# Kernel optimization log

Measured on AMD Instinct MI355X. Metric: run time of the kernel, lower is better.

Reference implementation:

```python
import jax, jax.numpy as jnp
import numpy as np

N_NODES = 50000
N_EDGES = 800000
F_IN = 128
HEADS = 2
C_HID = 64
N_GRAPHS = 32
NEG_SLOPE = 0.2
LP_LAYERS = 2
LP_ALPHA = 0.5


def gatv2_conv(x, src, dst, W_l, W_r, att, bias):
    """GATv2Conv (concat=True), edge_attr=None, self-loops already in src/dst."""
    H, C = att.shape
    N = x.shape[0]
    xl = (x @ W_l).reshape(N, H, C)  # source-side transform (x_j)
    xr = (x @ W_r).reshape(N, H, C)  # target-side transform (x_i)
    xj = xl[src]                      # [E,H,C]
    e = jax.nn.leaky_relu(xr[dst] + xj, NEG_SLOPE)
    logits = jnp.einsum('ehc,hc->eh', e, att)  # [E,H]
    # segment softmax over incoming edges of each target node
    m = jax.ops.segment_max(logits, dst, num_segments=N)
    m = jnp.where(jnp.isfinite(m), m, 0.0)
    p = jnp.exp(logits - m[dst])
    s = jax.ops.segment_sum(p, dst, num_segments=N)
    alpha = p / (s[dst] + 1e-16)
    out = jax.ops.segment_sum(xj * alpha[:, :, None], dst, num_segments=N)
    return out.reshape(N, H * C) + bias


def label_prop(y, src, dst):
    """PyG LabelPropagation: sym gcn_norm (no self-loops), clamp(0,1) post-step."""
    N = y.shape[0]
    ones = jnp.ones(src.shape[0], dtype=y.dtype)
    deg = jax.ops.segment_sum(ones, dst, num_segments=N)
    dinv = jnp.where(deg > 0, jax.lax.rsqrt(jnp.maximum(deg, 1.0)), 0.0)
    w = (dinv[src] * dinv[dst])[:, None]
    res = (1.0 - LP_ALPHA) * y
    out = y
    for _ in range(LP_LAYERS):
        out = LP_ALPHA * jax.ops.segment_sum(out[src] * w, dst, num_segments=N) + res
        out = jnp.clip(out, 0.0, 1.0)
    return out


def setup_inputs() -> dict:
    key = jax.random.key(0)
    ks = jax.random.split(key, 16)
    HC = HEADS * C_HID

    def glorot(k, shape):
        lim = np.sqrt(6.0 / (shape[0] + shape[-1]))
        return jax.random.uniform(k, shape, jnp.float32, -lim, lim)

    x = jax.random.normal(ks[0], (N_NODES, F_IN), jnp.float32)
    edge_index = jax.random.randint(ks[1], (2, N_EDGES), 0, N_NODES, jnp.int32)
    batch = jnp.sort(jax.random.randint(ks[2], (N_NODES,), 0, N_GRAPHS, jnp.int32))
    return {
        'x': x, 'edge_index': edge_index, 'batch': batch,
        'W_l1': glorot(ks[3], (F_IN, HC)), 'W_r1': glorot(ks[4], (F_IN, HC)),
        'att1': glorot(ks[5], (HEADS, C_HID)), 'b1': jnp.zeros((HC,), jnp.float32),
        'W_l2': glorot(ks[6], (HC, HC)), 'W_r2': glorot(ks[7], (HC, HC)),
        'att2': glorot(ks[8], (HEADS, C_HID)), 'b2': jnp.zeros((HC,), jnp.float32),
        'mlp_W1': glorot(ks[9], (F_IN + 2 * HC, 256)), 'mlp_b1': jnp.zeros((256,), jnp.float32),
        'mlp_W2': glorot(ks[10], (256, 128)), 'mlp_b2': jnp.zeros((128,), jnp.float32),
    }


def reference(x, edge_index, batch, W_l1, W_r1, att1, b1, W_l2, W_r2, att2, b2,
              mlp_W1, mlp_b1, mlp_W2, mlp_b2):
    N = x.shape[0]
    src, dst = edge_index[0], edge_index[1]
    # GATv2Conv adds self-loops by default
    loop = jnp.arange(N, dtype=src.dtype)
    src_sl = jnp.concatenate([src, loop])
    dst_sl = jnp.concatenate([dst, loop])

    h0 = x
    h1 = jax.nn.elu(gatv2_conv(h0, src_sl, dst_sl, W_l1, W_r1, att1, b1))
    h1 = label_prop(h1, src, dst)
    h2 = jax.nn.elu(gatv2_conv(h1, src_sl, dst_sl, W_l2, W_r2, att2, b2))
    h2 = label_prop(h2, src, dst)

    combined = jnp.concatenate([h0, h1, h2], axis=-1)  # [N, 384]
    # global mean pool over graphs
    sums = jax.ops.segment_sum(combined, batch, num_segments=N_GRAPHS)
    cnts = jax.ops.segment_sum(jnp.ones((N,), combined.dtype), batch, num_segments=N_GRAPHS)
    g = sums / jnp.maximum(cnts, 1.0)[:, None]  # [G, 384]

    h = jax.nn.relu(g @ mlp_W1 + mlp_b1)  # dropout is identity in eval
    return h @ mlp_W2 + mlp_b2
```

## Files before the change

### kernel.cpp

```cpp
#include <hip/hip_runtime.h>
#include <math.h>

#define FDIM 128
#define NEG_SLOPE 0.2f
#define LP_ALPHA 0.5f
#define NGRAPHS 32
#define POOLF 384
#define MLP_H 256
#define OUT_F 128
#define POOL_CH 8

#define LRELU(z) ((z) > 0.0f ? (z) : NEG_SLOPE * (z))
#define RFL(v) __builtin_amdgcn_readfirstlane(v)

__global__ void count_deg_k(const int* __restrict__ dst, int* __restrict__ deg, int E) {
    int e = blockIdx.x * blockDim.x + threadIdx.x;
    if (e < E) atomicAdd(&deg[dst[e]], 1);
}

__global__ __launch_bounds__(256) void scan_part_k(const int* __restrict__ deg,
                                                   int* __restrict__ tileSum, int N) {
    int b = blockIdx.x, t = threadIdx.x;
    int base = b * 1024 + t * 4;
    int v = 0;
    if (base + 3 < N) { int4 d = *(const int4*)(deg + base); v = d.x + d.y + d.z + d.w; }
    else if (base < N) {
        v = deg[base];
        if (base + 1 < N) v += deg[base + 1];
        if (base + 2 < N) v += deg[base + 2];
    }
#pragma unroll
    for (int off = 32; off > 0; off >>= 1) v += __shfl_xor(v, off, 64);
    __shared__ int ws[4];
    if ((t & 63) == 0) ws[t >> 6] = v;
    __syncthreads();
    if (t == 0) tileSum[b] = ws[0] + ws[1] + ws[2] + ws[3];
}

__global__ void scan_tiles_k(const int* __restrict__ tileSum, int* __restrict__ tileOff, int nt) {
    int t = threadIdx.x;
    int v = (t < nt) ? tileSum[t] : 0;
    int incl = v;
#pragma unroll
    for (int off = 1; off < 64; off <<= 1) {
        int u = __shfl_up(incl, off, 64);
        if (t >= off) incl += u;
    }
    if (t < nt) tileOff[t] = incl - v;
}

__global__ __launch_bounds__(256) void scan_write_k(const int* __restrict__ deg,
                                                    const int* __restrict__ tileOff,
                                                    int* __restrict__ row_ptr,
                                                    float* __restrict__ dinv, int N, int E) {
    int b = blockIdx.x, t = threadIdx.x;
    int base = b * 1024 + t * 4;
    int d0 = 0, d1 = 0, d2 = 0, d3 = 0;
    if (base + 3 < N) { int4 d = *(const int4*)(deg + base); d0 = d.x; d1 = d.y; d2 = d.z; d3 = d.w; }
    else if (base < N) {
        d0 = deg[base];
        if (base + 1 < N) d1 = deg[base + 1];
        if (base + 2 < N) d2 = deg[base + 2];
    }
    int lsum = d0 + d1 + d2 + d3;
    int lane = t & 63, wv = t >> 6;
    int incl = lsum;
#pragma unroll
    for (int off = 1; off < 64; off <<= 1) {
        int u = __shfl_up(incl, off, 64);
        if (lane >= off) incl += u;
    }
    __shared__ int wsum[4];
    if (lane == 63) wsum[wv] = incl;
    __syncthreads();
    int woff = 0;
#pragma unroll
    for (int k = 0; k < 4; ++k) if (k < wv) woff += wsum[k];
    int off0 = tileOff[b] + woff + (incl - lsum);
    if (base < N)     { row_ptr[base]     = off0;                dinv[base]     = d0 > 0 ? 1.0f / sqrtf((float)d0) : 0.0f; }
    if (base + 1 < N) { row_ptr[base + 1] = off0 + d0;           dinv[base + 1] = d1 > 0 ? 1.0f / sqrtf((float)d1) : 0.0f; }
    if (base + 2 < N) { row_ptr[base + 2] = off0 + d0 + d1;      dinv[base + 2] = d2 > 0 ? 1.0f / sqrtf((float)d2) : 0.0f; }
    if (base + 3 < N) { row_ptr[base + 3] = off0 + d0 + d1 + d2; dinv[base + 3] = d3 > 0 ? 1.0f / sqrtf((float)d3) : 0.0f; }
    if (b == 0 && t == 0) row_ptr[N] = E;
}

__global__ void scatter_k(const int* __restrict__ src, const int* __restrict__ dst,
                          const int* __restrict__ row_ptr, int* __restrict__ fill,
                          const float* __restrict__ dinv, int2* __restrict__ elist, int E) {
    int e = blockIdx.x * blockDim.x + threadIdx.x;
    if (e >= E) return;
    int d = dst[e], s = src[e];
    int pos = atomicAdd(&fill[d], 1);
    unsigned long long v = (unsigned int)s |
                           ((unsigned long long)(unsigned int)__float_as_int(dinv[s]) << 32);
    __builtin_nontemporal_store(v, (unsigned long long*)&elist[row_ptr[d] + pos]);
}

__global__ void gbound_k(const int* __restrict__ batch, int* __restrict__ gb, int N) {
    int g = threadIdx.x;
    if (g > NGRAPHS) return;
    int lo = 0, hi = N;
    while (lo < hi) {
        int mid = (lo + hi) >> 1;
        if (batch[mid] < g) lo = mid + 1; else hi = mid;
    }
    gb[g] = lo;
}

__global__ __launch_bounds__(256) void gemm128x2_k(const float* __restrict__ X,
                                                   const float* __restrict__ Wl,
                                                   const float* __restrict__ Wr,
                                                   float* __restrict__ Yl,
                                                   float* __restrict__ Yr, int N) {
    __shared__ float Xs[FDIM][68];
    int t = threadIdx.x;
    int r0 = blockIdx.x * 64;
    for (int idx = t; idx < 64 * FDIM; idx += 256) {
        int k = idx & 127, r = idx >> 7;
        int row = r0 + r;
        Xs[k][r] = (row < N) ? X[(size_t)row * FDIM + k] : 0.0f;
    }
    __syncthreads();
    int tr = t >> 5;
    int tc = t & 31;
    float accl[8][4] = {{0.f}}, accr[8][4] = {{0.f}};
#pragma unroll 2
    for (int k = 0; k < FDIM; ++k) {
        float4 bl = *(const float4*)(Wl + k * FDIM + tc * 4);
        float4 br = *(const float4*)(Wr + k * FDIM + tc * 4);
        float4 a0 = *(const float4*)(&Xs[k][tr * 8]);
        float4 a1 = *(const float4*)(&Xs[k][tr * 8 + 4]);
        float av[8] = {a0.x, a0.y, a0.z, a0.w, a1.x, a1.y, a1.z, a1.w};
#pragma unroll
        for (int r = 0; r < 8; ++r) {
            accl[r][0] = fmaf(av[r], bl.x, accl[r][0]);
            accl[r][1] = fmaf(av[r], bl.y, accl[r][1]);
            accl[r][2] = fmaf(av[r], bl.z, accl[r][2]);
            accl[r][3] = fmaf(av[r], bl.w, accl[r][3]);
            accr[r][0] = fmaf(av[r], br.x, accr[r][0]);
            accr[r][1] = fmaf(av[r], br.y, accr[r][1]);
            accr[r][2] = fmaf(av[r], br.z, accr[r][2]);
            accr[r][3] = fmaf(av[r], br.w, accr[r][3]);
        }
    }
#pragma unroll
    for (int r = 0; r < 8; ++r) {
        int row = r0 + tr * 8 + r;
        if (row < N) {
            *(float4*)(Yl + (size_t)row * FDIM + tc * 4) =
                make_float4(accl[r][0], accl[r][1], accl[r][2], accl[r][3]);
            *(float4*)(Yr + (size_t)row * FDIM + tc * 4) =
                make_float4(accr[r][0], accr[r][1], accr[r][2], accr[r][3]);
        }
    }
}

__global__ __launch_bounds__(256) void gat_pull_k(const float* __restrict__ xl,
                                                  const float* __restrict__ xr,
                                                  const int* __restrict__ row_ptr,
                                                  const int2* __restrict__ elist,
                                                  const float* __restrict__ att,
                                                  const float* __restrict__ bias,
                                                  float* __restrict__ out, int N) {
    int wid = threadIdx.x >> 6;
    int lane = threadIdx.x & 63;
    int i = blockIdx.x * 4 + wid;
    if (i >= N) return;
    float2 at  = *(const float2*)(att + 2 * lane);
    size_t ibase = (size_t)i * FDIM + 2 * lane;
    float2 xrv   = *(const float2*)(xr + ibase);
    float2 xself = *(const float2*)(xl + ibase);

    auto hred = [](float v) {
        v += __shfl_xor(v, 16, 64);
        v += __shfl_xor(v, 8, 64);
        v += __shfl_xor(v, 4, 64);
        v += __shfl_xor(v, 2, 64);
        v += __shfl_xor(v, 1, 64);
        return v;
    };

    float lself = hred(LRELU(xrv.x + xself.x) * at.x + LRELU(xrv.y + xself.y) * at.y);
    float m0 = lself, s0 = 1.0f, a0x = xself.x, a0y = xself.y;
    float m1 = -INFINITY, s1 = 0.0f, a1x = 0.0f, a1y = 0.0f;

    int beg = row_ptr[i], end = row_ptr[i + 1];
    int p = beg;
    for (; p + 3 < end; p += 4) {
        int j0 = RFL(elist[p].x);
        int j1 = RFL(elist[p + 1].x);
        int j2 = RFL(elist[p + 2].x);
        int j3 = RFL(elist[p + 3].x);
        float2 x0 = *(const float2*)(xl + (size_t)j0 * FDIM + 2 * lane);
        float2 x1 = *(const float2*)(xl + (size_t)j1 * FDIM + 2 * lane);
        float2 x2 = *(const float2*)(xl + (size_t)j2 * FDIM + 2 * lane);
        float2 x3 = *(const float2*)(xl + (size_t)j3 * FDIM + 2 * lane);
        float l0 = hred(LRELU(xrv.x + x0.x) * at.x + LRELU(xrv.y + x0.y) * at.y);
        float l1 = hred(LRELU(xrv.x + x1.x) * at.x + LRELU(xrv.y + x1.y) * at.y);
        float l2 = hred(LRELU(xrv.x + x2.x) * at.x + LRELU(xrv.y + x2.y) * at.y);
        float l3 = hred(LRELU(xrv.x + x3.x) * at.x + LRELU(xrv.y + x3.y) * at.y);
        { float mn = fmaxf(m0, l0); float sc = __expf(m0 - mn), pe = __expf(l0 - mn);
          s0 = fmaf(s0, sc, pe); a0x = fmaf(a0x, sc, pe * x0.x); a0y = fmaf(a0y, sc, pe * x0.y); m0 = mn; }
        { float mn = fmaxf(m1, l1); float sc = __expf(m1 - mn), pe = __expf(l1 - mn);
          s1 = fmaf(s1, sc, pe); a1x = fmaf(a1x, sc, pe * x1.x); a1y = fmaf(a1y, sc, pe * x1.y); m1 = mn; }
        { float mn = fmaxf(m0, l2); float sc = __expf(m0 - mn), pe = __expf(l2 - mn);
          s0 = fmaf(s0, sc, pe); a0x = fmaf(a0x, sc, pe * x2.x); a0y = fmaf(a0y, sc, pe * x2.y); m0 = mn; }
        { float mn = fmaxf(m1, l3); float sc = __expf(m1 - mn), pe = __expf(l3 - mn);
          s1 = fmaf(s1, sc, pe); a1x = fmaf(a1x, sc, pe * x3.x); a1y = fmaf(a1y, sc, pe * x3.y); m1 = mn; }
    }
    for (; p < end; ++p) {
        int j0 = RFL(elist[p].x);
        float2 x0 = *(const float2*)(xl + (size_t)j0 * FDIM + 2 * lane);
        float l0 = hred(LRELU(xrv.x + x0.x) * at.x + LRELU(xrv.y + x0.y) * at.y);
        float mn = fmaxf(m0, l0); float sc = __expf(m0 - mn), pe = __expf(l0 - mn);
        s0 = fmaf(s0, sc, pe); a0x = fmaf(a0x, sc, pe * x0.x); a0y = fmaf(a0y, sc, pe * x0.y); m0 = mn;
    }
    float mn = fmaxf(m0, m1);
    float c0 = __expf(m0 - mn);
    float c1 = (m1 == -INFINITY) ? 0.0f : __expf(m1 - mn);
    float s = fmaf(s0, c0, s1 * c1) + 1e-16f;
    float rx = (a0x * c0 + a1x * c1) / s;
    float ry = (a0y * c0 + a1y * c1) / s;
    float2 bv = *(const float2*)(bias + 2 * lane);
    float zx = rx + bv.x, zy = ry + bv.y;
    float2 o;
    o.x = (zx > 0.0f) ? zx : (__expf(zx) - 1.0f);
    o.y = (zy > 0.0f) ? zy : (__expf(zy) - 1.0f);
    *(float2*)(out + ibase) = o;
}

__global__ __launch_bounds__(256) void lp_pull_k(const float* __restrict__ y,
                                                 const float* __restrict__ cur,
                                                 float* __restrict__ nxt,
                                                 const int* __restrict__ row_ptr,
                                                 const int2* __restrict__ elist,
                                                 const float* __restrict__ dinv, int N) {
    int wid = threadIdx.x >> 6, lane = threadIdx.x & 63;
    int i = blockIdx.x * 4 + wid;
    if (i >= N) return;
    int beg = row_ptr[i], end = row_ptr[i + 1];
    float ax0 = 0.f, ay0 = 0.f, ax1 = 0.f, ay1 = 0.f;
    float ax2 = 0.f, ay2 = 0.f, ax3 = 0.f, ay3 = 0.f;
    float ax4 = 0.f, ay4 = 0.f, ax5 = 0.f, ay5 = 0.f;
    float ax6 = 0.f, ay6 = 0.f, ax7 = 0.f, ay7 = 0.f;
    int p = beg;
    for (; p + 7 < end; p += 8) {
        int2 e0 = elist[p + 0], e1 = elist[p + 1], e2 = elist[p + 2], e3 = elist[p + 3];
        int2 e4 = elist[p + 4], e5 = elist[p + 5], e6 = elist[p + 6], e7 = elist[p + 7];
        int j0 = RFL(e0.x); float w0 = __int_as_float(RFL(e0.y));
        int j1 = RFL(e1.x); float w1 = __int_as_float(RFL(e1.y));
        int j2 = RFL(e2.x); float w2 = __int_as_float(RFL(e2.y));
        int j3 = RFL(e3.x); float w3 = __int_as_float(RFL(e3.y));
        int j4 = RFL(e4.x); float w4 = __int_as_float(RFL(e4.y));
        int j5 = RFL(e5.x); float w5 = __int_as_float(RFL(e5.y));
        int j6 = RFL(e6.x); float w6 = __int_as_float(RFL(e6.y));
        int j7 = RFL(e7.x); float w7 = __int_as_float(RFL(e7.y));
        float2 v0 = *(const float2*)(cur + (size_t)j0 * FDIM + 2 * lane);
        float2 v1 = *(const float2*)(cur + (size_t)j1 * FDIM + 2 * lane);
        float2 v2 = *(const float2*)(cur + (size_t)j2 * FDIM + 2 * lane);
        float2 v3 = *(const float2*)(cur + (size_t)j3 * FDIM + 2 * lane);
        float2 v4 = *(const float2*)(cur + (size_t)j4 * FDIM + 2 * lane);
        float2 v5 = *(const float2*)(cur + (size_t)j5 * FDIM + 2 * lane);
        float2 v6 = *(const float2*)(cur + (size_t)j6 * FDIM + 2 * lane);
        float2 v7 = *(const float2*)(cur + (size_t)j7 * FDIM + 2 * lane);
        ax0 = fmaf(w0, v0.x, ax0); ay0 = fmaf(w0, v0.y, ay0);
        ax1 = fmaf(w1, v1.x, ax1); ay1 = fmaf(w1, v1.y, ay1);
        ax2 = fmaf(w2, v2.x, ax2); ay2 = fmaf(w2, v2.y, ay2);
        ax3 = fmaf(w3, v3.x, ax3); ay3 = fmaf(w3, v3.y, ay3);
        ax4 = fmaf(w4, v4.x, ax4); ay4 = fmaf(w4, v4.y, ay4);
        ax5 = fmaf(w5, v5.x, ax5); ay5 = fmaf(w5, v5.y, ay5);
        ax6 = fmaf(w6, v6.x, ax6); ay6 = fmaf(w6, v6.y, ay6);
        ax7 = fmaf(w7, v7.x, ax7); ay7 = fmaf(w7, v7.y, ay7);
    }
    for (; p < end; ++p) {
        int2 e0 = elist[p];
        int j0 = RFL(e0.x); float w0 = __int_as_float(RFL(e0.y));
        float2 v0 = *(const float2*)(cur + (size_t)j0 * FDIM + 2 * lane);
        ax0 = fmaf(w0, v0.x, ax0); ay0 = fmaf(w0, v0.y, ay0);
    }
    float sx = ((ax0 + ax1) + (ax2 + ax3)) + ((ax4 + ax5) + (ax6 + ax7));
    float sy = ((ay0 + ay1) + (ay2 + ay3)) + ((ay4 + ay5) + (ay6 + ay7));
    float di = dinv[i];
    float2 yv = *(const float2*)(y + (size_t)i * FDIM + 2 * lane);
    float vx = LP_ALPHA * (di * sx) + (1.0f - LP_ALPHA) * yv.x;
    float vy = LP_ALPHA * (di * sy) + (1.0f - LP_ALPHA) * yv.y;
    float2 o;
    o.x = fminf(fmaxf(vx, 0.f), 1.f);
    o.y = fminf(fmaxf(vy, 0.f), 1.f);
    *(float2*)(nxt + (size_t)i * FDIM + 2 * lane) = o;
}

__global__ void pool_part_k(const float* __restrict__ x, const float* __restrict__ h1,
                            const float* __restrict__ h2, const int* __restrict__ gb,
                            float* __restrict__ part) {
    int g = blockIdx.x, si = blockIdx.y, ch = blockIdx.z;
    int t = threadIdx.x;
    const float* s = (si == 0) ? x : ((si == 1) ? h1 : h2);
    int n0g = gb[g], n1g = gb[g + 1];
    int len = n1g - n0g;
    int per = (len + POOL_CH - 1) / POOL_CH;
    int n0 = n0g + ch * per;
    int n1 = min(n0 + per, n1g);
    float acc = 0.0f;
    for (int n = n0; n < n1; ++n) acc += s[(size_t)n * FDIM + t];
    part[(((g * 3 + si) << 3) + ch) * FDIM + t] = acc;
}

__global__ void mlp1_k(const float* __restrict__ part, const int* __restrict__ gb,
                       const float* __restrict__ W1, const float* __restrict__ b1,
                       float* __restrict__ h) {
    int g = blockIdx.x;
    int t = threadIdx.x;
    __shared__ float gm[POOLF];
    int cnt = gb[g + 1] - gb[g];
    float inv = 1.0f / fmaxf((float)cnt, 1.0f);
    for (int f = t; f < POOLF; f += 256) {
        int si = f >> 7, fl = f & 127;
        float s = 0.0f;
#pragma unroll
        for (int c = 0; c < POOL_CH; ++c)
            s += part[(((g * 3 + si) << 3) + c) * FDIM + fl];
        gm[f] = s * inv;
    }
    __syncthreads();
    float acc = b1[t];
    for (int k = 0; k < POOLF; ++k) acc = fmaf(gm[k], W1[k * MLP_H + t], acc);
    h[g * MLP_H + t] = fmaxf(acc, 0.0f);
}

__global__ void mlp2_k(const float* __restrict__ h, const float* __restrict__ W2,
                       const float* __restrict__ b2, float* __restrict__ out) {
    int g = blockIdx.x;
    int t = threadIdx.x;
    __shared__ float hs[MLP_H];
    for (int k = t; k < MLP_H; k += 128) hs[k] = h[g * MLP_H + k];
    __syncthreads();
    float acc = b2[t];
    for (int k = 0; k < MLP_H; ++k) acc = fmaf(hs[k], W2[k * OUT_F + t], acc);
    out[g * OUT_F + t] = acc;
}

extern "C" void kernel_launch(void* const* d_in, const int* in_sizes, int n_in,
                              void* d_out, int out_size, void* d_ws, size_t ws_size,
                              hipStream_t stream) {
    const float* x    = (const float*)d_in[0];
    const int*   ei   = (const int*)d_in[1];
    const int*   batch= (const int*)d_in[2];
    const float* W_l1 = (const float*)d_in[3];
    const float* W_r1 = (const float*)d_in[4];
    const float* att1 = (const float*)d_in[5];
    const float* b1   = (const float*)d_in[6];
    const float* W_l2 = (const float*)d_in[7];
    const float* W_r2 = (const float*)d_in[8];
    const float* att2 = (const float*)d_in[9];
    const float* b2   = (const float*)d_in[10];
    const float* mW1  = (const float*)d_in[11];
    const float* mb1  = (const float*)d_in[12];
    const float* mW2  = (const float*)d_in[13];
    const float* mb2  = (const float*)d_in[14];
    float* out = (float*)d_out;

    const int N = in_sizes[2];
    const int E = in_sizes[1] / 2;
    const int* src = ei;
    const int* dst = ei + E;

    char* w = (char*)d_ws;
    auto alloc = [&](size_t bytes) -> char* {
        char* p = w;
        w += (bytes + 255) & ~(size_t)255;
        return p;
    };
    float* bufA = (float*)alloc((size_t)N * FDIM * 4);
    float* bufB = (float*)alloc((size_t)N * FDIM * 4);
    float* bufC = (float*)alloc((size_t)N * FDIM * 4);
    float* bufD = (float*)alloc((size_t)N * FDIM * 4);
    int* deg     = (int*)alloc((size_t)N * 4);
    int* fill    = (int*)alloc((size_t)N * 4);
    int* row_lp  = (int*)alloc((size_t)(N + 1) * 4);
    int2* elist  = (int2*)alloc((size_t)E * 8);
    float* dinv  = (float*)alloc((size_t)N * 4);
    int* gb      = (int*)alloc((size_t)(NGRAPHS + 1) * 4);
    int* tileSum = (int*)alloc((size_t)64 * 4);
    int* tileOff = (int*)alloc((size_t)64 * 4);
    float* part  = (float*)alloc((size_t)NGRAPHS * 3 * POOL_CH * FDIM * 4);
    float* mlp_h = (float*)alloc((size_t)NGRAPHS * MLP_H * 4);

    const int TB = 256;
    int gE = (E + TB - 1) / TB;
    int nTiles = (N + 1023) / 1024;

    hipMemsetAsync(deg, 0, (size_t)N * 4, stream);
    hipMemsetAsync(fill, 0, (size_t)N * 4, stream);
    count_deg_k<<<gE, TB, 0, stream>>>(dst, deg, E);
    gbound_k<<<1, 64, 0, stream>>>(batch, gb, N);
    scan_part_k<<<nTiles, 256, 0, stream>>>(deg, tileSum, N);
    scan_tiles_k<<<1, 64, 0, stream>>>(tileSum, tileOff, nTiles);
    scan_write_k<<<nTiles, 256, 0, stream>>>(deg, tileOff, row_lp, dinv, N, E);
    scatter_k<<<gE, TB, 0, stream>>>(src, dst, row_lp, fill, dinv, elist, E);

    int gGemm = (N + 63) / 64;
    int gWave = (N + 3) / 4;

    gemm128x2_k<<<gGemm, 256, 0, stream>>>(x, W_l1, W_r1, bufA, bufB, N);
    gat_pull_k<<<gWave, 256, 0, stream>>>(bufA, bufB, row_lp, elist, att1, b1, bufC, N);
    lp_pull_k<<<gWave, 256, 0, stream>>>(bufC, bufC, bufA, row_lp, elist, dinv, N);
    lp_pull_k<<<gWave, 256, 0, stream>>>(bufC, bufA, bufC, row_lp, elist, dinv, N);

    gemm128x2_k<<<gGemm, 256, 0, stream>>>(bufC, W_l2, W_r2, bufA, bufB, N);
    gat_pull_k<<<gWave, 256, 0, stream>>>(bufA, bufB, row_lp, elist, att2, b2, bufD, N);
    lp_pull_k<<<gWave, 256, 0, stream>>>(bufD, bufD, bufA, row_lp, elist, dinv, N);
    lp_pull_k<<<gWave, 256, 0, stream>>>(bufD, bufA, bufD, row_lp, elist, dinv, N);

    pool_part_k<<<dim3(NGRAPHS, 3, POOL_CH), 128, 0, stream>>>(x, bufC, bufD, gb, part);

    mlp1_k<<<NGRAPHS, 256, 0, stream>>>(part, gb, mW1, mb1, mlp_h);
    mlp2_k<<<NGRAPHS, 128, 0, stream>>>(mlp_h, mW2, mb2, out);
}
```

Before: 773.5 us.

## Split each wave into two half-waves processing separate edges with float4 gathers

The GAT and label-propagation pull kernels now give each 32-lane half of a wave its own set of edges, with each lane loading float4 feature slices. The halves' online-softmax or sum partials are merged with a cross-half shuffle at the end. This doubles the number of independent row gathers in flight per wave and widens each load, at the cost of extra shuffles, predicated tail handling and one idle half during the store. Separately, the scatter step now uses a cursor array initialised with the row offsets, which removes one memset and the row_ptr lookup.

```diff
diff --git a/kernel.cpp b/kernel.cpp
--- a/kernel.cpp
+++ b/kernel.cpp
@@ -11,7 +11,6 @@
 #define POOL_CH 8
 
 #define LRELU(z) ((z) > 0.0f ? (z) : NEG_SLOPE * (z))
-#define RFL(v) __builtin_amdgcn_readfirstlane(v)
 
 __global__ void count_deg_k(const int* __restrict__ dst, int* __restrict__ deg, int E) {
     int e = blockIdx.x * blockDim.x + threadIdx.x;
@@ -52,6 +51,7 @@
 __global__ __launch_bounds__(256) void scan_write_k(const int* __restrict__ deg,
                                                     const int* __restrict__ tileOff,
                                                     int* __restrict__ row_ptr,
+                                                    int* __restrict__ cursor,
                                                     float* __restrict__ dinv, int N, int E) {
     int b = blockIdx.x, t = threadIdx.x;
     int base = b * 1024 + t * 4;
@@ -77,23 +77,27 @@
 #pragma unroll
     for (int k = 0; k < 4; ++k) if (k < wv) woff += wsum[k];
     int off0 = tileOff[b] + woff + (incl - lsum);
-    if (base < N)     { row_ptr[base]     = off0;                dinv[base]     = d0 > 0 ? 1.0f / sqrtf((float)d0) : 0.0f; }
-    if (base + 1 < N) { row_ptr[base + 1] = off0 + d0;           dinv[base + 1] = d1 > 0 ? 1.0f / sqrtf((float)d1) : 0.0f; }
-    if (base + 2 < N) { row_ptr[base + 2] = off0 + d0 + d1;      dinv[base + 2] = d2 > 0 ? 1.0f / sqrtf((float)d2) : 0.0f; }
-    if (base + 3 < N) { row_ptr[base + 3] = off0 + d0 + d1 + d2; dinv[base + 3] = d3 > 0 ? 1.0f / sqrtf((float)d3) : 0.0f; }
+    if (base < N)     { row_ptr[base]     = off0;                cursor[base]     = off0;
+                        dinv[base]     = d0 > 0 ? 1.0f / sqrtf((float)d0) : 0.0f; }
+    if (base + 1 < N) { row_ptr[base + 1] = off0 + d0;           cursor[base + 1] = off0 + d0;
+                        dinv[base + 1] = d1 > 0 ? 1.0f / sqrtf((float)d1) : 0.0f; }
+    if (base + 2 < N) { row_ptr[base + 2] = off0 + d0 + d1;      cursor[base + 2] = off0 + d0 + d1;
+                        dinv[base + 2] = d2 > 0 ? 1.0f / sqrtf((float)d2) : 0.0f; }
+    if (base + 3 < N) { row_ptr[base + 3] = off0 + d0 + d1 + d2; cursor[base + 3] = off0 + d0 + d1 + d2;
+                        dinv[base + 3] = d3 > 0 ? 1.0f / sqrtf((float)d3) : 0.0f; }
     if (b == 0 && t == 0) row_ptr[N] = E;
 }
 
 __global__ void scatter_k(const int* __restrict__ src, const int* __restrict__ dst,
-                          const int* __restrict__ row_ptr, int* __restrict__ fill,
-                          const float* __restrict__ dinv, int2* __restrict__ elist, int E) {
+                          int* __restrict__ cursor, const float* __restrict__ dinv,
+                          int2* __restrict__ elist, int E) {
     int e = blockIdx.x * blockDim.x + threadIdx.x;
     if (e >= E) return;
     int d = dst[e], s = src[e];
-    int pos = atomicAdd(&fill[d], 1);
+    int pos = atomicAdd(&cursor[d], 1);
     unsigned long long v = (unsigned int)s |
                            ((unsigned long long)(unsigned int)__float_as_int(dinv[s]) << 32);
-    __builtin_nontemporal_store(v, (unsigned long long*)&elist[row_ptr[d] + pos]);
+    __builtin_nontemporal_store(v, (unsigned long long*)&elist[pos]);
 }
 
 __global__ void gbound_k(const int* __restrict__ batch, int* __restrict__ gb, int N) {
@@ -164,15 +168,18 @@
                                                   float* __restrict__ out, int N) {
     int wid = threadIdx.x >> 6;
     int lane = threadIdx.x & 63;
+    int half = lane >> 5;
+    int lh = lane & 31;
     int i = blockIdx.x * 4 + wid;
     if (i >= N) return;
-    float2 at  = *(const float2*)(att + 2 * lane);
-    size_t ibase = (size_t)i * FDIM + 2 * lane;
-    float2 xrv   = *(const float2*)(xr + ibase);
-    float2 xself = *(const float2*)(xl + ibase);
-
-    auto hred = [](float v) {
-        v += __shfl_xor(v, 16, 64);
+    float4 at = *(const float4*)(att + 4 * lh);
+    size_t ibase = (size_t)i * FDIM + 4 * lh;
+    float4 xrv = *(const float4*)(xr + ibase);
+    float4 xs  = *(const float4*)(xl + ibase);
+
+    auto qdot = [&](float4 xv) {
+        float v = LRELU(xrv.x + xv.x) * at.x + LRELU(xrv.y + xv.y) * at.y
+                + LRELU(xrv.z + xv.z) * at.z + LRELU(xrv.w + xv.w) * at.w;
         v += __shfl_xor(v, 8, 64);
         v += __shfl_xor(v, 4, 64);
         v += __shfl_xor(v, 2, 64);
@@ -180,53 +187,73 @@
         return v;
     };
 
-    float lself = hred(LRELU(xrv.x + xself.x) * at.x + LRELU(xrv.y + xself.y) * at.y);
-    float m0 = lself, s0 = 1.0f, a0x = xself.x, a0y = xself.y;
-    float m1 = -INFINITY, s1 = 0.0f, a1x = 0.0f, a1y = 0.0f;
+    float lself = qdot(xs);
+    float m0 = half ? -INFINITY : lself;
+    float s0 = half ? 0.0f : 1.0f;
+    float4 a0 = half ? make_float4(0.f, 0.f, 0.f, 0.f) : xs;
+    float m1 = -INFINITY, s1 = 0.0f;
+    float4 a1 = make_float4(0.f, 0.f, 0.f, 0.f);
 
     int beg = row_ptr[i], end = row_ptr[i + 1];
-    int p = beg;
-    for (; p + 3 < end; p += 4) {
-        int j0 = RFL(elist[p].x);
-        int j1 = RFL(elist[p + 1].x);
-        int j2 = RFL(elist[p + 2].x);
-        int j3 = RFL(elist[p + 3].x);
-        float2 x0 = *(const float2*)(xl + (size_t)j0 * FDIM + 2 * lane);
-        float2 x1 = *(const float2*)(xl + (size_t)j1 * FDIM + 2 * lane);
-        float2 x2 = *(const float2*)(xl + (size_t)j2 * FDIM + 2 * lane);
-        float2 x3 = *(const float2*)(xl + (size_t)j3 * FDIM + 2 * lane);
-        float l0 = hred(LRELU(xrv.x + x0.x) * at.x + LRELU(xrv.y + x0.y) * at.y);
-        float l1 = hred(LRELU(xrv.x + x1.x) * at.x + LRELU(xrv.y + x1.y) * at.y);
-        float l2 = hred(LRELU(xrv.x + x2.x) * at.x + LRELU(xrv.y + x2.y) * at.y);
-        float l3 = hred(LRELU(xrv.x + x3.x) * at.x + LRELU(xrv.y + x3.y) * at.y);
-        { float mn = fmaxf(m0, l0); float sc = __expf(m0 - mn), pe = __expf(l0 - mn);
-          s0 = fmaf(s0, sc, pe); a0x = fmaf(a0x, sc, pe * x0.x); a0y = fmaf(a0y, sc, pe * x0.y); m0 = mn; }
-        { float mn = fmaxf(m1, l1); float sc = __expf(m1 - mn), pe = __expf(l1 - mn);
-          s1 = fmaf(s1, sc, pe); a1x = fmaf(a1x, sc, pe * x1.x); a1y = fmaf(a1y, sc, pe * x1.y); m1 = mn; }
-        { float mn = fmaxf(m0, l2); float sc = __expf(m0 - mn), pe = __expf(l2 - mn);
-          s0 = fmaf(s0, sc, pe); a0x = fmaf(a0x, sc, pe * x2.x); a0y = fmaf(a0y, sc, pe * x2.y); m0 = mn; }
-        { float mn = fmaxf(m1, l3); float sc = __expf(m1 - mn), pe = __expf(l3 - mn);
-          s1 = fmaf(s1, sc, pe); a1x = fmaf(a1x, sc, pe * x3.x); a1y = fmaf(a1y, sc, pe * x3.y); m1 = mn; }
-    }
-    for (; p < end; ++p) {
-        int j0 = RFL(elist[p].x);
-        float2 x0 = *(const float2*)(xl + (size_t)j0 * FDIM + 2 * lane);
-        float l0 = hred(LRELU(xrv.x + x0.x) * at.x + LRELU(xrv.y + x0.y) * at.y);
-        float mn = fmaxf(m0, l0); float sc = __expf(m0 - mn), pe = __expf(l0 - mn);
-        s0 = fmaf(s0, sc, pe); a0x = fmaf(a0x, sc, pe * x0.x); a0y = fmaf(a0y, sc, pe * x0.y); m0 = mn;
-    }
-    float mn = fmaxf(m0, m1);
-    float c0 = __expf(m0 - mn);
-    float c1 = (m1 == -INFINITY) ? 0.0f : __expf(m1 - mn);
-    float s = fmaf(s0, c0, s1 * c1) + 1e-16f;
-    float rx = (a0x * c0 + a1x * c1) / s;
-    float ry = (a0y * c0 + a1y * c1) / s;
-    float2 bv = *(const float2*)(bias + 2 * lane);
-    float zx = rx + bv.x, zy = ry + bv.y;
-    float2 o;
-    o.x = (zx > 0.0f) ? zx : (__expf(zx) - 1.0f);
-    o.y = (zy > 0.0f) ? zy : (__expf(zy) - 1.0f);
-    *(float2*)(out + ibase) = o;
+    for (int p = beg; p < end; p += 4) {
+        int i0 = p + half, i1 = p + 2 + half;
+        bool v0 = i0 < end, v1 = i1 < end;
+        int j0 = elist[min(i0, end - 1)].x;
+        int j1 = elist[min(i1, end - 1)].x;
+        float4 x0 = *(const float4*)(xl + (size_t)j0 * FDIM + 4 * lh);
+        float4 x1 = *(const float4*)(xl + (size_t)j1 * FDIM + 4 * lh);
+        float l0 = qdot(x0);
+        float l1 = qdot(x1);
+        if (v0) {
+            float mn = fmaxf(m0, l0);
+            float sc = __expf(m0 - mn), pe = __expf(l0 - mn);
+            s0 = fmaf(s0, sc, pe);
+            a0.x = fmaf(a0.x, sc, pe * x0.x); a0.y = fmaf(a0.y, sc, pe * x0.y);
+            a0.z = fmaf(a0.z, sc, pe * x0.z); a0.w = fmaf(a0.w, sc, pe * x0.w);
+            m0 = mn;
+        }
+        if (v1) {
+            float mn = fmaxf(m1, l1);
+            float sc = __expf(m1 - mn), pe = __expf(l1 - mn);
+            s1 = fmaf(s1, sc, pe);
+            a1.x = fmaf(a1.x, sc, pe * x1.x); a1.y = fmaf(a1.y, sc, pe * x1.y);
+            a1.z = fmaf(a1.z, sc, pe * x1.z); a1.w = fmaf(a1.w, sc, pe * x1.w);
+            m1 = mn;
+        }
+    }
+    {
+        float mn = fmaxf(m0, m1);
+        float c0 = (m0 == -INFINITY) ? 0.0f : __expf(m0 - mn);
+        float c1 = (m1 == -INFINITY) ? 0.0f : __expf(m1 - mn);
+        s0 = s0 * c0 + s1 * c1;
+        a0.x = a0.x * c0 + a1.x * c1; a0.y = a0.y * c0 + a1.y * c1;
+        a0.z = a0.z * c0 + a1.z * c1; a0.w = a0.w * c0 + a1.w * c1;
+        m0 = mn;
+    }
+    {
+        float pm = __shfl_xor(m0, 32, 64);
+        float ps = __shfl_xor(s0, 32, 64);
+        float px = __shfl_xor(a0.x, 32, 64), py = __shfl_xor(a0.y, 32, 64);
+        float pz = __shfl_xor(a0.z, 32, 64), pw = __shfl_xor(a0.w, 32, 64);
+        float mn = fmaxf(m0, pm);
+        float c0 = (m0 == -INFINITY) ? 0.0f : __expf(m0 - mn);
+        float c1 = (pm == -INFINITY) ? 0.0f : __expf(pm - mn);
+        s0 = s0 * c0 + ps * c1;
+        a0.x = a0.x * c0 + px * c1; a0.y = a0.y * c0 + py * c1;
+        a0.z = a0.z * c0 + pz * c1; a0.w = a0.w * c0 + pw * c1;
+    }
+    if (half == 0) {
+        float inv = 1.0f / (s0 + 1e-16f);
+        float4 bv = *(const float4*)(bias + 4 * lh);
+        float zx = a0.x * inv + bv.x, zy = a0.y * inv + bv.y;
+        float zz = a0.z * inv + bv.z, zw = a0.w * inv + bv.w;
+        float4 o;
+        o.x = (zx > 0.0f) ? zx : (__expf(zx) - 1.0f);
+        o.y = (zy > 0.0f) ? zy : (__expf(zy) - 1.0f);
+        o.z = (zz > 0.0f) ? zz : (__expf(zz) - 1.0f);
+        o.w = (zw > 0.0f) ? zw : (__expf(zw) - 1.0f);
+        *(float4*)(out + ibase) = o;
+    }
 }
 
 __global__ __launch_bounds__(256) void lp_pull_k(const float* __restrict__ y,
@@ -236,58 +263,54 @@
                                                  const int2* __restrict__ elist,
                                                  const float* __restrict__ dinv, int N) {
     int wid = threadIdx.x >> 6, lane = threadIdx.x & 63;
+    int half = lane >> 5, lh = lane & 31;
     int i = blockIdx.x * 4 + wid;
     if (i >= N) return;
     int beg = row_ptr[i], end = row_ptr[i + 1];
-    float ax0 = 0.f, ay0 = 0.f, ax1 = 0.f, ay1 = 0.f;
-    float ax2 = 0.f, ay2 = 0.f, ax3 = 0.f, ay3 = 0.f;
-    float ax4 = 0.f, ay4 = 0.f, ax5 = 0.f, ay5 = 0.f;
-    float ax6 = 0.f, ay6 = 0.f, ax7 = 0.f, ay7 = 0.f;
-    int p = beg;
-    for (; p + 7 < end; p += 8) {
-        int2 e0 = elist[p + 0], e1 = elist[p + 1], e2 = elist[p + 2], e3 = elist[p + 3];
-        int2 e4 = elist[p + 4], e5 = elist[p + 5], e6 = elist[p + 6], e7 = elist[p + 7];
-        int j0 = RFL(e0.x); float w0 = __int_as_float(RFL(e0.y));
-        int j1 = RFL(e1.x); float w1 = __int_as_float(RFL(e1.y));
-        int j2 = RFL(e2.x); float w2 = __int_as_float(RFL(e2.y));
-        int j3 = RFL(e3.x); float w3 = __int_as_float(RFL(e3.y));
-        int j4 = RFL(e4.x); float w4 = __int_as_float(RFL(e4.y));
-        int j5 = RFL(e5.x); float w5 = __int_as_float(RFL(e5.y));
-        int j6 = RFL(e6.x); float w6 = __int_as_float(RFL(e6.y));
-        int j7 = RFL(e7.x); float w7 = __int_as_float(RFL(e7.y));
-        float2 v0 = *(const float2*)(cur + (size_t)j0 * FDIM + 2 * lane);
-        float2 v1 = *(const float2*)(cur + (size_t)j1 * FDIM + 2 * lane);
-        float2 v2 = *(const float2*)(cur + (size_t)j2 * FDIM + 2 * lane);
-        float2 v3 = *(const float2*)(cur + (size_t)j3 * FDIM + 2 * lane);
-        float2 v4 = *(const float2*)(cur + (size_t)j4 * FDIM + 2 * lane);
-        float2 v5 = *(const float2*)(cur + (size_t)j5 * FDIM + 2 * lane);
-        float2 v6 = *(const float2*)(cur + (size_t)j6 * FDIM + 2 * lane);
-        float2 v7 = *(const float2*)(cur + (size_t)j7 * FDIM + 2 * lane);
-        ax0 = fmaf(w0, v0.x, ax0); ay0 = fmaf(w0, v0.y, ay0);
-        ax1 = fmaf(w1, v1.x, ax1); ay1 = fmaf(w1, v1.y, ay1);
-        ax2 = fmaf(w2, v2.x, ax2); ay2 = fmaf(w2, v2.y, ay2);
-        ax3 = fmaf(w3, v3.x, ax3); ay3 = fmaf(w3, v3.y, ay3);
-        ax4 = fmaf(w4, v4.x, ax4); ay4 = fmaf(w4, v4.y, ay4);
-        ax5 = fmaf(w5, v5.x, ax5); ay5 = fmaf(w5, v5.y, ay5);
-        ax6 = fmaf(w6, v6.x, ax6); ay6 = fmaf(w6, v6.y, ay6);
-        ax7 = fmaf(w7, v7.x, ax7); ay7 = fmaf(w7, v7.y, ay7);
-    }
-    for (; p < end; ++p) {
-        int2 e0 = elist[p];
-        int j0 = RFL(e0.x); float w0 = __int_as_float(RFL(e0.y));
-        float2 v0 = *(const float2*)(cur + (size_t)j0 * FDIM + 2 * lane);
-        ax0 = fmaf(w0, v0.x, ax0); ay0 = fmaf(w0, v0.y, ay0);
-    }
-    float sx = ((ax0 + ax1) + (ax2 + ax3)) + ((ax4 + ax5) + (ax6 + ax7));
-    float sy = ((ay0 + ay1) + (ay2 + ay3)) + ((ay4 + ay5) + (ay6 + ay7));
-    float di = dinv[i];
-    float2 yv = *(const float2*)(y + (size_t)i * FDIM + 2 * lane);
-    float vx = LP_ALPHA * (di * sx) + (1.0f - LP_ALPHA) * yv.x;
-    float vy = LP_ALPHA * (di * sy) + (1.0f - LP_ALPHA) * yv.y;
-    float2 o;
-    o.x = fminf(fmaxf(vx, 0.f), 1.f);
-    o.y = fminf(fmaxf(vy, 0.f), 1.f);
-    *(float2*)(nxt + (size_t)i * FDIM + 2 * lane) = o;
+    float4 a0 = make_float4(0.f, 0.f, 0.f, 0.f), a1 = a0, a2 = a0, a3 = a0;
+    for (int p = beg; p < end; p += 8) {
+        int i0 = p + half, i1 = p + 2 + half, i2 = p + 4 + half, i3 = p + 6 + half;
+        int2 e0 = elist[min(i0, end - 1)];
+        int2 e1 = elist[min(i1, end - 1)];
+        int2 e2 = elist[min(i2, end - 1)];
+        int2 e3 = elist[min(i3, end - 1)];
+        float w0 = (i0 < end) ? __int_as_float(e0.y) : 0.0f;
+        float w1 = (i1 < end) ? __int_as_float(e1.y) : 0.0f;
+        float w2 = (i2 < end) ? __int_as_float(e2.y) : 0.0f;
+        float w3 = (i3 < end) ? __int_as_float(e3.y) : 0.0f;
+        float4 x0 = *(const float4*)(cur + (size_t)e0.x * FDIM + 4 * lh);
+        float4 x1 = *(const float4*)(cur + (size_t)e1.x * FDIM + 4 * lh);
+        float4 x2 = *(const float4*)(cur + (size_t)e2.x * FDIM + 4 * lh);
+        float4 x3 = *(const float4*)(cur + (size_t)e3.x * FDIM + 4 * lh);
+        a0.x = fmaf(w0, x0.x, a0.x); a0.y = fmaf(w0, x0.y, a0.y);
+        a0.z = fmaf(w0, x0.z, a0.z); a0.w = fmaf(w0, x0.w, a0.w);
+        a1.x = fmaf(w1, x1.x, a1.x); a1.y = fmaf(w1, x1.y, a1.y);
+        a1.z = fmaf(w1, x1.z, a1.z); a1.w = fmaf(w1, x1.w, a1.w);
+        a2.x = fmaf(w2, x2.x, a2.x); a2.y = fmaf(w2, x2.y, a2.y);
+        a2.z = fmaf(w2, x2.z, a2.z); a2.w = fmaf(w2, x2.w, a2.w);
+        a3.x = fmaf(w3, x3.x, a3.x); a3.y = fmaf(w3, x3.y, a3.y);
+        a3.z = fmaf(w3, x3.z, a3.z); a3.w = fmaf(w3, x3.w, a3.w);
+    }
+    float4 a;
+    a.x = (a0.x + a1.x) + (a2.x + a3.x);
+    a.y = (a0.y + a1.y) + (a2.y + a3.y);
+    a.z = (a0.z + a1.z) + (a2.z + a3.z);
+    a.w = (a0.w + a1.w) + (a2.w + a3.w);
+    a.x += __shfl_xor(a.x, 32, 64);
+    a.y += __shfl_xor(a.y, 32, 64);
+    a.z += __shfl_xor(a.z, 32, 64);
+    a.w += __shfl_xor(a.w, 32, 64);
+    if (half == 0) {
+        float di = dinv[i];
+        size_t ibase = (size_t)i * FDIM + 4 * lh;
+        float4 yv = *(const float4*)(y + ibase);
+        float4 o;
+        o.x = fminf(fmaxf(fmaf(LP_ALPHA * di, a.x, (1.0f - LP_ALPHA) * yv.x), 0.f), 1.f);
+        o.y = fminf(fmaxf(fmaf(LP_ALPHA * di, a.y, (1.0f - LP_ALPHA) * yv.y), 0.f), 1.f);
+        o.z = fminf(fmaxf(fmaf(LP_ALPHA * di, a.z, (1.0f - LP_ALPHA) * yv.z), 0.f), 1.f);
+        o.w = fminf(fmaxf(fmaf(LP_ALPHA * di, a.w, (1.0f - LP_ALPHA) * yv.w), 0.f), 1.f);
+        *(float4*)(nxt + ibase) = o;
+    }
 }
 
 __global__ void pool_part_k(const float* __restrict__ x, const float* __restrict__ h1,
@@ -376,7 +399,7 @@
     float* bufC = (float*)alloc((size_t)N * FDIM * 4);
     float* bufD = (float*)alloc((size_t)N * FDIM * 4);
     int* deg     = (int*)alloc((size_t)N * 4);
-    int* fill    = (int*)alloc((size_t)N * 4);
+    int* cursor  = (int*)alloc((size_t)N * 4);
     int* row_lp  = (int*)alloc((size_t)(N + 1) * 4);
     int2* elist  = (int2*)alloc((size_t)E * 8);
     float* dinv  = (float*)alloc((size_t)N * 4);
@@ -391,13 +414,12 @@
     int nTiles = (N + 1023) / 1024;
 
     hipMemsetAsync(deg, 0, (size_t)N * 4, stream);
-    hipMemsetAsync(fill, 0, (size_t)N * 4, stream);
     count_deg_k<<<gE, TB, 0, stream>>>(dst, deg, E);
     gbound_k<<<1, 64, 0, stream>>>(batch, gb, N);
     scan_part_k<<<nTiles, 256, 0, stream>>>(deg, tileSum, N);
     scan_tiles_k<<<1, 64, 0, stream>>>(tileSum, tileOff, nTiles);
-    scan_write_k<<<nTiles, 256, 0, stream>>>(deg, tileOff, row_lp, dinv, N, E);
-    scatter_k<<<gE, TB, 0, stream>>>(src, dst, row_lp, fill, dinv, elist, E);
+    scan_write_k<<<nTiles, 256, 0, stream>>>(deg, tileOff, row_lp, cursor, dinv, N, E);
+    scatter_k<<<gE, TB, 0, stream>>>(src, dst, cursor, dinv, elist, E);
 
     int gGemm = (N + 63) / 64;
     int gWave = (N + 3) / 4;
```

After: 739.0 us. -4.5%, faster.
